# Kernel optimization log

Hardware: AMD Instinct MI355X
Metric: run time of the kernel (lower is better)

## Reference

```python
import jax, jax.numpy as jnp
import numpy as np

N, H, F = 131072, 256, 4096
MIN_FRAG = 3
LN_EPS = 1e-5
NORM_EPS = 1e-12
CONSISTENCY_FACTOR = 0.03
INTERMOLECULAR_WEIGHT = 0.2
SCALING_FACTOR = 0.05  # initial_strength at epoch 0 (progressive schedule, eval mode)


def _normalize(x):
    # torch F.normalize(p=2, dim=1): x / max(||x||, eps)
    n = jnp.linalg.norm(x, axis=-1, keepdims=True)
    return x / jnp.maximum(n, NORM_EPS)


def _frag_consistency(feat, frag_ids, valid):
    # size-weighted sum of per-fragment mean deviations == mean deviation over valid atoms
    m = valid.astype(feat.dtype)[:, None]
    seg_sum = jax.ops.segment_sum(feat * m, frag_ids, num_segments=F)
    seg_cnt = jax.ops.segment_sum(m, frag_ids, num_segments=F)
    means = seg_sum / jnp.maximum(seg_cnt, 1.0)  # scatter-mean over valid atoms
    sim = jnp.sum(_normalize(feat) * _normalize(means)[frag_ids], axis=-1)  # [N]
    dev = (1.0 - sim) * valid.astype(feat.dtype)
    return jnp.sum(dev) / jnp.maximum(jnp.sum(valid.astype(feat.dtype)), 1.0)


def setup_inputs() -> dict:
    key = jax.random.key(0)
    ks = jax.random.split(key, 8)
    return {
        "scalar_short": jax.random.normal(ks[0], (N, H), jnp.float32),
        "scalar_long": jax.random.normal(ks[1], (N, H), jnp.float32),
        "vector_short": jax.random.normal(ks[2], (N, 3, H), jnp.float32),
        "vector_long": jax.random.normal(ks[3], (N, 3, H), jnp.float32),
        "fragment_ids": jax.random.randint(ks[4], (N,), 0, F, dtype=jnp.int32),
        "ln_gamma": jnp.ones((H,), jnp.float32),
        "ln_beta": jnp.zeros((H,), jnp.float32),
        "W1": jax.random.normal(ks[5], (H, H), jnp.float32) / np.sqrt(H),
        "b1": jnp.zeros((H,), jnp.float32),
        "Wv": jax.random.normal(ks[6], (H, H), jnp.float32) / np.sqrt(H),
    }


def reference(scalar_short, scalar_long, vector_short, vector_long, fragment_ids,
              ln_gamma, ln_beta, W1, b1, Wv):
    # valid_mask: atoms belonging to fragments of size >= MIN_FRAG
    sizes = jax.ops.segment_sum(jnp.ones((N,), jnp.float32), fragment_ids, num_segments=F)
    valid = sizes[fragment_ids] >= MIN_FRAG  # [N] bool

    # scalar_projector: LayerNorm -> Linear -> SiLU (dropout identity at eval)
    mu = jnp.mean(scalar_short, axis=-1, keepdims=True)
    var = jnp.var(scalar_short, axis=-1, keepdims=True)
    xh = (scalar_short - mu) / jnp.sqrt(var + LN_EPS) * ln_gamma + ln_beta
    scalar_features = jax.nn.silu(xh @ W1.T + b1)  # [N, H]

    intra = _frag_consistency(scalar_features, fragment_ids, valid)

    # vector branch: per-atom magnitude = mean over 3 spatial comps of ||.||_2 over hidden
    vec_mag = jnp.mean(jnp.linalg.norm(vector_short, axis=2), axis=1, keepdims=True)  # [N,1]
    # Linear(bias=False) on mag.expand(-1,H) then [:, :1] == silu(mag * sum(Wv[0,:]))
    w0 = jnp.sum(Wv[0])
    vector_features = jax.nn.silu(vec_mag * w0)  # [N,1]
    vec_loss = _frag_consistency(vector_features, fragment_ids, valid)

    # interfragment differentiation over ALL atoms (no valid mask)
    cnt = jax.ops.segment_sum(jnp.ones((N, 1), jnp.float32), fragment_ids, num_segments=F)
    sfrag = jax.ops.segment_sum(scalar_features, fragment_ids, num_segments=F) / jnp.maximum(cnt, 1.0)
    vfrag = jax.ops.segment_sum(vec_mag, fragment_ids, num_segments=F) / jnp.maximum(cnt, 1.0)
    combined = _normalize(jnp.concatenate([sfrag, vfrag], axis=1))  # [F, H+1]
    sim = combined @ combined.T  # [F, F]
    off_sum = jnp.sum(sim) - jnp.trace(sim)
    inter = off_sum / (F * F - F + 1e-6)

    total = intra + vec_loss + INTERMOLECULAR_WEIGHT * inter
    return CONSISTENCY_FACTOR * total * SCALING_FACTOR
```

## Files before the change

kernel.cpp:

```cpp
#include <hip/hip_runtime.h>
#include <hip/hip_bf16.h>
#include <stdint.h>

#define NA 131072
#define HD 256
#define NF 4096
#define MINFRAG 3
#define LN_EPS 1e-5f
#define NEPS 1e-12f

#define OFF_CNT    0ull
#define OFF_VSUM   16384ull
#define OFF_VFSUM  32768ull
#define OFF_NVSUM  49152ull
#define OFF_FILL   65536ull
#define OFF_DBL    81920ull
#define OFF_SSUM   86016ull
#define OFF_NSUM   4280320ull
#define ZERO_BYTES 8474624ull
#define OFF_OFFS   8474624ull
#define OFF_SVEC   8491008ull
#define OFF_C0     8492032ull
#define OFF_W0     8493056ull
#define OFF_GBF    8493568ull
#define OFF_ORDER  8624640ull

#define IDX_TRACE 257
#define IDX_DEVS  258
#define IDX_DEVV  259
#define IDX_VCNT  260

typedef __attribute__((ext_vector_type(8))) short short8;
typedef __attribute__((ext_vector_type(4))) float f32x4;
union F4S8 { float4 f; short8 s; };
union BFU { __hip_bfloat16 b; unsigned short u; };

__device__ __forceinline__ unsigned short f2b(float x) {
    BFU t; t.b = __float2bfloat16(x); return t.u;
}
__device__ __forceinline__ float b2f(unsigned short u) {
    return __uint_as_float(((uint32_t)u) << 16);
}
__device__ __forceinline__ float silu_f(float x) { return x / (1.f + expf(-x)); }

__global__ __launch_bounds__(256) void k_prep(
    const float* __restrict__ W1, const float* __restrict__ gamma,
    const float* __restrict__ beta, const float* __restrict__ b1,
    const float* __restrict__ Wv,
    unsigned short* __restrict__ Gbf, float* __restrict__ svec,
    float* __restrict__ c0, float* __restrict__ w0) {
    __shared__ float red[8];
    int o = blockIdx.x;
    int t = threadIdx.x;
    if (o < HD) {
        float w = W1[(size_t)o * HD + t];
        unsigned short gb = f2b(w * gamma[t]);
        Gbf[(size_t)o * HD + t] = gb;
        float sp = b2f(gb);
        float cp = w * beta[t];
#pragma unroll
        for (int m = 32; m; m >>= 1) { sp += __shfl_xor(sp, m, 64); cp += __shfl_xor(cp, m, 64); }
        int wv = t >> 6;
        if ((t & 63) == 0) { red[wv] = sp; red[4 + wv] = cp; }
        __syncthreads();
        if (t == 0) {
            svec[o] = red[0] + red[1] + red[2] + red[3];
            c0[o]   = red[4] + red[5] + red[6] + red[7] + b1[o];
        }
    } else {
        float v = Wv[t];
#pragma unroll
        for (int m = 32; m; m >>= 1) v += __shfl_xor(v, m, 64);
        int wv = t >> 6;
        if ((t & 63) == 0) red[wv] = v;
        __syncthreads();
        if (t == 0) w0[0] = red[0] + red[1] + red[2] + red[3];
    }
}

__global__ __launch_bounds__(256) void k_stats(
    const float* __restrict__ vs, const int* __restrict__ fid,
    const float* __restrict__ w0p,
    int* __restrict__ cnt, float* __restrict__ vsum,
    float* __restrict__ vfsum, float* __restrict__ nvsum) {
    int gwave = (blockIdx.x * blockDim.x + threadIdx.x) >> 6;
    int lane = threadIdx.x & 63;
    int nw = (gridDim.x * blockDim.x) >> 6;
    float w0 = w0p[0];
    for (int i = gwave; i < NA; i += nw) {
        const float* base = vs + (size_t)i * 3 * HD;
        float4 v0 = ((const float4*)(base))[lane];
        float4 v1 = ((const float4*)(base + HD))[lane];
        float4 v2 = ((const float4*)(base + 2 * HD))[lane];
        float q0 = v0.x * v0.x + v0.y * v0.y + v0.z * v0.z + v0.w * v0.w;
        float q1 = v1.x * v1.x + v1.y * v1.y + v1.z * v1.z + v1.w * v1.w;
        float q2 = v2.x * v2.x + v2.y * v2.y + v2.z * v2.z + v2.w * v2.w;
#pragma unroll
        for (int m = 32; m; m >>= 1) {
            q0 += __shfl_xor(q0, m, 64);
            q1 += __shfl_xor(q1, m, 64);
            q2 += __shfl_xor(q2, m, 64);
        }
        if (lane == 0) {
            float vm = (sqrtf(q0) + sqrtf(q1) + sqrtf(q2)) * (1.f / 3.f);
            float vf = silu_f(vm * w0);
            float nv = vf / fmaxf(fabsf(vf), NEPS);
            int f = fid[i];
            atomicAdd(&cnt[f], 1);
            atomicAdd(&vsum[f], vm);
            atomicAdd(&vfsum[f], vf);
            atomicAdd(&nvsum[f], nv);
        }
    }
}

__global__ __launch_bounds__(256) void k_scan(const int* __restrict__ cnt,
                                              int* __restrict__ offs) {
    __shared__ int wsum[4];
    int t = threadIdx.x;
    int base = t * 16;
    int c[16];
    int tot = 0;
#pragma unroll
    for (int j = 0; j < 16; ++j) { c[j] = cnt[base + j]; tot += c[j]; }
    int lane = t & 63, w = t >> 6;
    int v = tot;
#pragma unroll
    for (int d = 1; d < 64; d <<= 1) {
        int o = __shfl_up(v, d, 64);
        if (lane >= d) v += o;
    }
    if (lane == 63) wsum[w] = v;
    __syncthreads();
    int wbase = 0;
    for (int i = 0; i < w; ++i) wbase += wsum[i];
    int run = wbase + v - tot;
#pragma unroll
    for (int j = 0; j < 16; ++j) { offs[base + j] = run; run += c[j]; }
}

__global__ __launch_bounds__(256) void k_scatter(
    const int* __restrict__ fid, const int* __restrict__ offs,
    int* __restrict__ fill, int* __restrict__ order) {
    int i = blockIdx.x * blockDim.x + threadIdx.x;
    if (i < NA) {
        int f = fid[i];
        int p = atomicAdd(&fill[f], 1);
        order[offs[f] + p] = i;
    }
}

__global__ __launch_bounds__(256) void k_gemm(
    const float* __restrict__ A, const unsigned short* __restrict__ Gbf,
    const float* __restrict__ svec, const float* __restrict__ c0,
    const int* __restrict__ order, const int* __restrict__ fid,
    const int* __restrict__ offs, const int* __restrict__ cnt,
    float* __restrict__ ssum, float* __restrict__ nsum) {
    __shared__ float4 As16[64 * 8];
    __shared__ float4 Bs16[256 * 8];
    __shared__ float muS[64], rsS[64], rnS[64];
    __shared__ float sqL[64][4];
    __shared__ int fragS[64];

    int tid = threadIdx.x;
    int lane = tid & 63, wid = tid >> 6;
    int r0 = blockIdx.x * 64;
    int rowT = tid >> 4;
    int c4 = tid & 15;

    if (tid < 64) {
        int gi = order[r0 + tid];
        muS[tid] = __int_as_float(gi);
        fragS[tid] = fid[gi];
    }
    __syncthreads();
    int rid[4];
#pragma unroll
    for (int p = 0; p < 4; ++p) rid[p] = __float_as_int(muS[16 * p + rowT]);
    __syncthreads();

    f32x4 acc[4][4] = {};
    float s1p[4] = {0, 0, 0, 0}, s2p[4] = {0, 0, 0, 0};

    for (int k0 = 0; k0 < HD; k0 += 64) {
#pragma unroll
        for (int p = 0; p < 4; ++p) {
            int row = 16 * p + rowT;
            float4 v = *(const float4*)(A + (size_t)rid[p] * HD + k0 + c4 * 4);
            s1p[p] += v.x + v.y + v.z + v.w;
            s2p[p] += v.x * v.x + v.y * v.y + v.z * v.z + v.w * v.w;
            ushort4 pk;
            pk.x = f2b(v.x); pk.y = f2b(v.y); pk.z = f2b(v.z); pk.w = f2b(v.w);
            int slot = row * 8 + ((c4 >> 1) ^ (row & 7));
            ((ushort4*)&As16[slot])[c4 & 1] = pk;
        }
#pragma unroll
        for (int p = 0; p < 8; ++p) {
            int u = p * 256 + tid;
            int n = u >> 3, cc = u & 7;
            float4 g = *(const float4*)(Gbf + (size_t)n * HD + k0 + cc * 8);
            Bs16[n * 8 + (cc ^ (n & 7))] = g;
        }
        __syncthreads();
#pragma unroll
        for (int kk = 0; kk < 2; ++kk) {
            int uo = kk * 4 + (lane >> 4);
            short8 a[4], b[4];
#pragma unroll
            for (int mi = 0; mi < 4; ++mi) {
                int r = mi * 16 + (lane & 15);
                F4S8 t_; t_.f = As16[r * 8 + (uo ^ (r & 7))];
                a[mi] = t_.s;
            }
#pragma unroll
            for (int ni = 0; ni < 4; ++ni) {
                int n = wid * 64 + ni * 16 + (lane & 15);
                F4S8 t_; t_.f = Bs16[n * 8 + (uo ^ (n & 7))];
                b[ni] = t_.s;
            }
#pragma unroll
            for (int mi = 0; mi < 4; ++mi)
#pragma unroll
                for (int ni = 0; ni < 4; ++ni)
                    acc[mi][ni] = __builtin_amdgcn_mfma_f32_16x16x32_bf16(
                        a[mi], b[ni], acc[mi][ni], 0, 0, 0);
        }
        __syncthreads();
    }
#pragma unroll
    for (int p = 0; p < 4; ++p) {
        float s1 = s1p[p], s2 = s2p[p];
#pragma unroll
        for (int m = 1; m < 16; m <<= 1) {
            s1 += __shfl_xor(s1, m, 64);
            s2 += __shfl_xor(s2, m, 64);
        }
        if (c4 == 0) {
            int row = 16 * p + rowT;
            float mu_ = s1 * (1.f / HD);
            float var = s2 * (1.f / HD) - mu_ * mu_;
            muS[row] = mu_;
            rsS[row] = rsqrtf(var + LN_EPS);
        }
    }
    __syncthreads();
    float sv[4], cv[4];
#pragma unroll
    for (int ni = 0; ni < 4; ++ni) {
        int c = wid * 64 + ni * 16 + (lane & 15);
        sv[ni] = svec[c];
        cv[ni] = c0[c];
    }
    unsigned short* featS = (unsigned short*)Bs16;
    float sq[4][4];
#pragma unroll
    for (int mi = 0; mi < 4; ++mi)
#pragma unroll
        for (int q = 0; q < 4; ++q) {
            int rl = mi * 16 + (lane >> 4) * 4 + q;
            float mu_ = muS[rl], rs_ = rsS[rl];
            float sqa = 0.f;
#pragma unroll
            for (int ni = 0; ni < 4; ++ni) {
                int c = wid * 64 + ni * 16 + (lane & 15);
                float pre = rs_ * (acc[mi][ni][q] - mu_ * sv[ni]) + cv[ni];
                unsigned short us = f2b(silu_f(pre));
                featS[rl * 256 + (c ^ ((rl & 7) << 2))] = us;
                float fr = b2f(us);
                sqa += fr * fr;
            }
            sq[mi][q] = sqa;
        }
#pragma unroll
    for (int mi = 0; mi < 4; ++mi)
#pragma unroll
        for (int q = 0; q < 4; ++q) {
            float s_ = sq[mi][q];
            s_ += __shfl_xor(s_, 1, 64);
            s_ += __shfl_xor(s_, 2, 64);
            s_ += __shfl_xor(s_, 4, 64);
            s_ += __shfl_xor(s_, 8, 64);
            if ((lane & 15) == 0) sqL[mi * 16 + (lane >> 4) * 4 + q][wid] = s_;
        }
    __syncthreads();
    if (tid < 64) {
        float t = sqL[tid][0] + sqL[tid][1] + sqL[tid][2] + sqL[tid][3];
        rnS[tid] = 1.f / fmaxf(sqrtf(t), NEPS);
    }
    __syncthreads();
    int cc = wid * 64 + lane;
    float sAcc = 0.f, nAcc = 0.f;
    int curF = fragS[0];
    for (int row = 0; row < 64; ++row) {
        int f = fragS[row];
        if (f != curF) {
            int gs = offs[curF], n = cnt[curF];
            if (gs >= r0 && gs + n <= r0 + 64) {
                ssum[(size_t)curF * HD + cc] = sAcc;
                nsum[(size_t)curF * HD + cc] = nAcc;
            } else {
                atomicAdd(&ssum[(size_t)curF * HD + cc], sAcc);
                atomicAdd(&nsum[(size_t)curF * HD + cc], nAcc);
            }
            sAcc = 0.f; nAcc = 0.f; curF = f;
        }
        float v = b2f(featS[row * 256 + (cc ^ ((row & 7) << 2))]);
        sAcc += v;
        nAcc = fmaf(v, rnS[row], nAcc);
    }
    {
        int gs = offs[curF], n = cnt[curF];
        if (gs >= r0 && gs + n <= r0 + 64) {
            ssum[(size_t)curF * HD + cc] = sAcc;
            nsum[(size_t)curF * HD + cc] = nAcc;
        } else {
            atomicAdd(&ssum[(size_t)curF * HD + cc], sAcc);
            atomicAdd(&nsum[(size_t)curF * HD + cc], nAcc);
        }
    }
}

__global__ __launch_bounds__(256) void k_frag(
    const float* __restrict__ ssum, const float* __restrict__ nsum,
    const int* __restrict__ cnt, const float* __restrict__ vsum,
    const float* __restrict__ vfsum, const float* __restrict__ nvsum,
    double* __restrict__ dbl) {
    int gwave = (blockIdx.x * blockDim.x + threadIdx.x) >> 6;
    int lane = threadIdx.x & 63;
    int nw = (gridDim.x * blockDim.x) >> 6;

    double la0 = 0, la1 = 0, la2 = 0, la3 = 0;
    double lv = 0, ltr = 0, lvc = 0, ldS = 0, ldV = 0;

    for (int f = gwave; f < NF; f += nw) {
        float4 s = ((const float4*)(ssum + (size_t)f * HD))[lane];
        float4 nn = ((const float4*)(nsum + (size_t)f * HD))[lane];
        int c = cnt[f];
        float ssq = s.x * s.x + s.y * s.y + s.z * s.z + s.w * s.w;
        float dsn = nn.x * s.x + nn.y * s.y + nn.z * s.z + nn.w * s.w;
#pragma unroll
        for (int m = 32; m; m >>= 1) {
            ssq += __shfl_xor(ssq, m, 64);
            dsn += __shfl_xor(dsn, m, 64);
        }
        float inv_all = 1.f / fmaxf((float)c, 1.f);
        float m0 = s.x * inv_all, m1 = s.y * inv_all, m2 = s.z * inv_all, m3 = s.w * inv_all;
        float ssq_mean = ssq * inv_all * inv_all;
        float vfr = vsum[f] * inv_all;
        float nrm2 = ssq_mean + vfr * vfr;
        float inv = 1.f / fmaxf(sqrtf(nrm2), NEPS);
        la0 += (double)(m0 * inv);
        la1 += (double)(m1 * inv);
        la2 += (double)(m2 * inv);
        la3 += (double)(m3 * inv);
        if (lane == 0) {
            lv += (double)(vfr * inv);
            ltr += (double)(nrm2 * inv * inv);
            if (c >= MINFRAG) {
                lvc += (double)c;
                float denom = fmaxf(sqrtf(ssq), NEPS);
                ldS += (double)c - (double)(dsn / denom);
                float vfm = vfsum[f] * inv_all;
                float vsgn = vfm / fmaxf(fabsf(vfm), NEPS);
                ldV += (double)c - (double)(vsgn * nvsum[f]);
            }
        }
    }
    atomicAdd(&dbl[4 * lane + 0], la0);
    atomicAdd(&dbl[4 * lane + 1], la1);
    atomicAdd(&dbl[4 * lane + 2], la2);
    atomicAdd(&dbl[4 * lane + 3], la3);
    if (lane == 0) {
        atomicAdd(&dbl[256], lv);
        atomicAdd(&dbl[IDX_TRACE], ltr);
        atomicAdd(&dbl[IDX_VCNT], lvc);
        atomicAdd(&dbl[IDX_DEVS], ldS);
        atomicAdd(&dbl[IDX_DEVV], ldV);
    }
}

__global__ __launch_bounds__(64) void k_final(const double* __restrict__ dbl,
                                              float* __restrict__ out) {
    if (threadIdx.x == 0 && blockIdx.x == 0) {
        double s2 = 0;
        for (int d = 0; d < 257; ++d) s2 += dbl[d] * dbl[d];
        double off = s2 - dbl[IDX_TRACE];
        double inter = off / ((double)NF * NF - NF + 1e-6);
        double vc = fmax(dbl[IDX_VCNT], 1.0);
        double total = dbl[IDX_DEVS] / vc + dbl[IDX_DEVV] / vc + 0.2 * inter;
        out[0] = (float)(0.03 * 0.05 * total);
    }
}

extern "C" void kernel_launch(void* const* d_in, const int* in_sizes, int n_in,
                              void* d_out, int out_size, void* d_ws, size_t ws_size,
                              hipStream_t stream) {
    const float* scalar_short = (const float*)d_in[0];
    const float* vector_short = (const float*)d_in[2];
    const int* fragment_ids = (const int*)d_in[4];
    const float* ln_gamma = (const float*)d_in[5];
    const float* ln_beta = (const float*)d_in[6];
    const float* W1 = (const float*)d_in[7];
    const float* b1 = (const float*)d_in[8];
    const float* Wv = (const float*)d_in[9];
    float* out = (float*)d_out;

    char* ws = (char*)d_ws;
    int* cnt = (int*)(ws + OFF_CNT);
    float* vsum = (float*)(ws + OFF_VSUM);
    float* vfsum = (float*)(ws + OFF_VFSUM);
    float* nvsum = (float*)(ws + OFF_NVSUM);
    int* fill = (int*)(ws + OFF_FILL);
    double* dbl = (double*)(ws + OFF_DBL);
    float* ssum = (float*)(ws + OFF_SSUM);
    float* nsum = (float*)(ws + OFF_NSUM);
    int* offs = (int*)(ws + OFF_OFFS);
    float* svec = (float*)(ws + OFF_SVEC);
    float* c0 = (float*)(ws + OFF_C0);
    float* w0 = (float*)(ws + OFF_W0);
    unsigned short* Gbf = (unsigned short*)(ws + OFF_GBF);
    int* order = (int*)(ws + OFF_ORDER);

    hipMemsetAsync(ws, 0, ZERO_BYTES, stream);
    k_prep<<<HD + 1, 256, 0, stream>>>(W1, ln_gamma, ln_beta, b1, Wv, Gbf, svec, c0, w0);
    k_stats<<<2048, 256, 0, stream>>>(vector_short, fragment_ids, w0, cnt, vsum, vfsum, nvsum);
    k_scan<<<1, 256, 0, stream>>>(cnt, offs);
    k_scatter<<<NA / 256, 256, 0, stream>>>(fragment_ids, offs, fill, order);
    k_gemm<<<NA / 64, 256, 0, stream>>>(scalar_short, Gbf, svec, c0, order,
                                        fragment_ids, offs, cnt, ssum, nsum);
    k_frag<<<64, 256, 0, stream>>>(ssum, nsum, cnt, vsum, vfsum, nvsum, dbl);
    k_final<<<1, 64, 0, stream>>>(dbl, out);
}
```

Measured before the change: 252.7 us.

## Fuse vector-magnitude stats into sorted GEMM and drop large memset

The separate pass over vector_short that computed per-atom magnitudes and per-fragment sums is folded into the GEMM kernel. Each block now reads its fragment-sorted atoms' vector rows alongside the scalar tile, so that streaming overlaps with MFMA work and one launch goes away. The GEMM tile grows to 128 rows with 512 threads. W1·gamma is pre-swizzled into the shared-memory layout so the B tile loads become straight vector copies. Zeroing of the large ssum/nsum buffers moves from a memset into a new histogram kernel, which now also builds the fragment counts. In exchange the fused kernel has higher register and shared-memory pressure, and the vector rows are gathered in sorted order instead of read sequentially.

Result: slower. 292.6 us (+15.8%).

```diff
diff --git a/kernel.cpp b/kernel.cpp
--- a/kernel.cpp
+++ b/kernel.cpp
@@ -15,15 +15,15 @@
 #define OFF_NVSUM  49152ull
 #define OFF_FILL   65536ull
 #define OFF_DBL    81920ull
-#define OFF_SSUM   86016ull
-#define OFF_NSUM   4280320ull
-#define ZERO_BYTES 8474624ull
-#define OFF_OFFS   8474624ull
-#define OFF_SVEC   8491008ull
-#define OFF_C0     8492032ull
-#define OFF_W0     8493056ull
-#define OFF_GBF    8493568ull
-#define OFF_ORDER  8624640ull
+#define ZERO_HEAD  84224ull
+#define OFF_OFFS   86016ull
+#define OFF_SVEC   102400ull
+#define OFF_C0     103424ull
+#define OFF_W0     104448ull
+#define OFF_GBF    106496ull
+#define OFF_ORDER  237568ull
+#define OFF_SSUM   761856ull
+#define OFF_NSUM   4956160ull
 
 #define IDX_TRACE 257
 #define IDX_DEVS  258
@@ -47,7 +47,7 @@
     const float* __restrict__ W1, const float* __restrict__ gamma,
     const float* __restrict__ beta, const float* __restrict__ b1,
     const float* __restrict__ Wv,
-    unsigned short* __restrict__ Gbf, float* __restrict__ svec,
+    unsigned short* __restrict__ GbfArr, float* __restrict__ svec,
     float* __restrict__ c0, float* __restrict__ w0) {
     __shared__ float red[8];
     int o = blockIdx.x;
@@ -55,7 +55,8 @@
     if (o < HD) {
         float w = W1[(size_t)o * HD + t];
         unsigned short gb = f2b(w * gamma[t]);
-        Gbf[(size_t)o * HD + t] = gb;
+        int kc = t >> 6, cc = (t >> 3) & 7, klo = t & 7;
+        GbfArr[(size_t)kc * 16384 + (o * 8 + (cc ^ (o & 7))) * 8 + klo] = gb;
         float sp = b2f(gb);
         float cp = w * beta[t];
 #pragma unroll
@@ -78,40 +79,12 @@
     }
 }
 
-__global__ __launch_bounds__(256) void k_stats(
-    const float* __restrict__ vs, const int* __restrict__ fid,
-    const float* __restrict__ w0p,
-    int* __restrict__ cnt, float* __restrict__ vsum,
-    float* __restrict__ vfsum, float* __restrict__ nvsum) {
-    int gwave = (blockIdx.x * blockDim.x + threadIdx.x) >> 6;
-    int lane = threadIdx.x & 63;
-    int nw = (gridDim.x * blockDim.x) >> 6;
-    float w0 = w0p[0];
-    for (int i = gwave; i < NA; i += nw) {
-        const float* base = vs + (size_t)i * 3 * HD;
-        float4 v0 = ((const float4*)(base))[lane];
-        float4 v1 = ((const float4*)(base + HD))[lane];
-        float4 v2 = ((const float4*)(base + 2 * HD))[lane];
-        float q0 = v0.x * v0.x + v0.y * v0.y + v0.z * v0.z + v0.w * v0.w;
-        float q1 = v1.x * v1.x + v1.y * v1.y + v1.z * v1.z + v1.w * v1.w;
-        float q2 = v2.x * v2.x + v2.y * v2.y + v2.z * v2.z + v2.w * v2.w;
-#pragma unroll
-        for (int m = 32; m; m >>= 1) {
-            q0 += __shfl_xor(q0, m, 64);
-            q1 += __shfl_xor(q1, m, 64);
-            q2 += __shfl_xor(q2, m, 64);
-        }
-        if (lane == 0) {
-            float vm = (sqrtf(q0) + sqrtf(q1) + sqrtf(q2)) * (1.f / 3.f);
-            float vf = silu_f(vm * w0);
-            float nv = vf / fmaxf(fabsf(vf), NEPS);
-            int f = fid[i];
-            atomicAdd(&cnt[f], 1);
-            atomicAdd(&vsum[f], vm);
-            atomicAdd(&vfsum[f], vf);
-            atomicAdd(&nvsum[f], nv);
-        }
-    }
+__global__ __launch_bounds__(256) void k_hist(
+    const int* __restrict__ fid, int* __restrict__ cnt, float4* __restrict__ zbuf) {
+    int i = blockIdx.x * 256 + threadIdx.x;
+    float4 z = {0.f, 0.f, 0.f, 0.f};
+    zbuf[i] = z;
+    if (i < NA) atomicAdd(&cnt[fid[i]], 1);
 }
 
 __global__ __launch_bounds__(256) void k_scan(const int* __restrict__ cnt,
@@ -150,56 +123,84 @@
     }
 }
 
-__global__ __launch_bounds__(256) void k_gemm(
-    const float* __restrict__ A, const unsigned short* __restrict__ Gbf,
+#define BM 128
+__global__ __launch_bounds__(512, 2) void k_gemm(
+    const float* __restrict__ A, const unsigned short* __restrict__ GbfArr,
     const float* __restrict__ svec, const float* __restrict__ c0,
+    const float* __restrict__ vs, const float* __restrict__ w0p,
     const int* __restrict__ order, const int* __restrict__ fid,
     const int* __restrict__ offs, const int* __restrict__ cnt,
+    float* __restrict__ vsum, float* __restrict__ vfsum, float* __restrict__ nvsum,
     float* __restrict__ ssum, float* __restrict__ nsum) {
-    __shared__ float4 As16[64 * 8];
-    __shared__ float4 Bs16[256 * 8];
-    __shared__ float muS[64], rsS[64], rnS[64];
-    __shared__ float sqL[64][4];
-    __shared__ int fragS[64];
+    __shared__ char U[65536];
+    __shared__ float muS[BM], rsS[BM], rnS[BM];
+    __shared__ float sqL[BM][4];
+    __shared__ int ridS[BM], fragS[BM];
+
+    float4* As = (float4*)U;
+    float4* Bs = (float4*)(U + 16384);
+    unsigned short* featS = (unsigned short*)U;
 
     int tid = threadIdx.x;
     int lane = tid & 63, wid = tid >> 6;
-    int r0 = blockIdx.x * 64;
-    int rowT = tid >> 4;
-    int c4 = tid & 15;
-
-    if (tid < 64) {
+    int wr = wid >> 2, wc = wid & 3;
+    int r0 = blockIdx.x * BM;
+    int rowA = tid >> 2, sub = tid & 3;
+    float w0 = w0p[0];
+
+    if (tid < BM) {
         int gi = order[r0 + tid];
-        muS[tid] = __int_as_float(gi);
+        ridS[tid] = gi;
         fragS[tid] = fid[gi];
     }
     __syncthreads();
-    int rid[4];
-#pragma unroll
-    for (int p = 0; p < 4; ++p) rid[p] = __float_as_int(muS[16 * p + rowT]);
-    __syncthreads();
 
     f32x4 acc[4][4] = {};
-    float s1p[4] = {0, 0, 0, 0}, s2p[4] = {0, 0, 0, 0};
-
-    for (int k0 = 0; k0 < HD; k0 += 64) {
+    float s1 = 0.f, s2 = 0.f;
+    const float* Ap = A + (size_t)ridS[rowA] * HD + sub * 16;
+
+    for (int kc = 0; kc < 4; ++kc) {
 #pragma unroll
         for (int p = 0; p < 4; ++p) {
-            int row = 16 * p + rowT;
-            float4 v = *(const float4*)(A + (size_t)rid[p] * HD + k0 + c4 * 4);
-            s1p[p] += v.x + v.y + v.z + v.w;
-            s2p[p] += v.x * v.x + v.y * v.y + v.z * v.z + v.w * v.w;
+            int idx = p * 512 + tid;
+            Bs[idx] = *(const float4*)(GbfArr + (size_t)kc * 16384 + (size_t)idx * 8);
+        }
+#pragma unroll
+        for (int q = 0; q < 4; ++q) {
+            int f4 = sub * 4 + q;
+            float4 v = *(const float4*)(Ap + kc * 64 + q * 4);
+            s1 += v.x + v.y + v.z + v.w;
+            s2 += v.x * v.x + v.y * v.y + v.z * v.z + v.w * v.w;
             ushort4 pk;
             pk.x = f2b(v.x); pk.y = f2b(v.y); pk.z = f2b(v.z); pk.w = f2b(v.w);
-            int slot = row * 8 + ((c4 >> 1) ^ (row & 7));
-            ((ushort4*)&As16[slot])[c4 & 1] = pk;
-        }
-#pragma unroll
-        for (int p = 0; p < 8; ++p) {
-            int u = p * 256 + tid;
-            int n = u >> 3, cc = u & 7;
-            float4 g = *(const float4*)(Gbf + (size_t)n * HD + k0 + cc * 8);
-            Bs16[n * 8 + (cc ^ (n & 7))] = g;
+            ((ushort4*)&As[rowA * 8 + ((f4 >> 1) ^ (rowA & 7))])[f4 & 1] = pk;
+        }
+#pragma unroll
+        for (int j = 0; j < 4; ++j) {
+            int lr = kc * 32 + wid * 4 + j;
+            int gi = ridS[lr];
+            const float* vb = vs + (size_t)gi * 3 * HD;
+            float4 v0 = ((const float4*)vb)[lane];
+            float4 v1 = ((const float4*)(vb + HD))[lane];
+            float4 v2 = ((const float4*)(vb + 2 * HD))[lane];
+            float q0 = v0.x * v0.x + v0.y * v0.y + v0.z * v0.z + v0.w * v0.w;
+            float q1 = v1.x * v1.x + v1.y * v1.y + v1.z * v1.z + v1.w * v1.w;
+            float q2 = v2.x * v2.x + v2.y * v2.y + v2.z * v2.z + v2.w * v2.w;
+#pragma unroll
+            for (int m = 32; m; m >>= 1) {
+                q0 += __shfl_xor(q0, m, 64);
+                q1 += __shfl_xor(q1, m, 64);
+                q2 += __shfl_xor(q2, m, 64);
+            }
+            if (lane == 0) {
+                float vm = (sqrtf(q0) + sqrtf(q1) + sqrtf(q2)) * (1.f / 3.f);
+                float vf = silu_f(vm * w0);
+                float nv = vf / fmaxf(fabsf(vf), NEPS);
+                int f = fragS[lr];
+                atomicAdd(&vsum[f], vm);
+                atomicAdd(&vfsum[f], vf);
+                atomicAdd(&nvsum[f], nv);
+            }
         }
         __syncthreads();
 #pragma unroll
@@ -208,14 +209,14 @@
             short8 a[4], b[4];
 #pragma unroll
             for (int mi = 0; mi < 4; ++mi) {
-                int r = mi * 16 + (lane & 15);
-                F4S8 t_; t_.f = As16[r * 8 + (uo ^ (r & 7))];
+                int r = wr * 64 + mi * 16 + (lane & 15);
+                F4S8 t_; t_.f = As[r * 8 + (uo ^ (r & 7))];
                 a[mi] = t_.s;
             }
 #pragma unroll
             for (int ni = 0; ni < 4; ++ni) {
-                int n = wid * 64 + ni * 16 + (lane & 15);
-                F4S8 t_; t_.f = Bs16[n * 8 + (uo ^ (n & 7))];
+                int n = wc * 64 + ni * 16 + (lane & 15);
+                F4S8 t_; t_.f = Bs[n * 8 + (uo ^ (n & 7))];
                 b[ni] = t_.s;
             }
 #pragma unroll
@@ -227,42 +228,33 @@
         }
         __syncthreads();
     }
-#pragma unroll
-    for (int p = 0; p < 4; ++p) {
-        float s1 = s1p[p], s2 = s2p[p];
-#pragma unroll
-        for (int m = 1; m < 16; m <<= 1) {
-            s1 += __shfl_xor(s1, m, 64);
-            s2 += __shfl_xor(s2, m, 64);
-        }
-        if (c4 == 0) {
-            int row = 16 * p + rowT;
-            float mu_ = s1 * (1.f / HD);
-            float var = s2 * (1.f / HD) - mu_ * mu_;
-            muS[row] = mu_;
-            rsS[row] = rsqrtf(var + LN_EPS);
-        }
+    s1 += __shfl_xor(s1, 1, 64); s1 += __shfl_xor(s1, 2, 64);
+    s2 += __shfl_xor(s2, 1, 64); s2 += __shfl_xor(s2, 2, 64);
+    if (sub == 0) {
+        float mu_ = s1 * (1.f / HD);
+        float var = s2 * (1.f / HD) - mu_ * mu_;
+        muS[rowA] = mu_;
+        rsS[rowA] = rsqrtf(var + LN_EPS);
     }
     __syncthreads();
     float sv[4], cv[4];
 #pragma unroll
     for (int ni = 0; ni < 4; ++ni) {
-        int c = wid * 64 + ni * 16 + (lane & 15);
+        int c = wc * 64 + ni * 16 + (lane & 15);
         sv[ni] = svec[c];
         cv[ni] = c0[c];
     }
-    unsigned short* featS = (unsigned short*)Bs16;
     float sq[4][4];
 #pragma unroll
     for (int mi = 0; mi < 4; ++mi)
 #pragma unroll
         for (int q = 0; q < 4; ++q) {
-            int rl = mi * 16 + (lane >> 4) * 4 + q;
+            int rl = wr * 64 + mi * 16 + (lane >> 4) * 4 + q;
             float mu_ = muS[rl], rs_ = rsS[rl];
             float sqa = 0.f;
 #pragma unroll
             for (int ni = 0; ni < 4; ++ni) {
-                int c = wid * 64 + ni * 16 + (lane & 15);
+                int c = wc * 64 + ni * 16 + (lane & 15);
                 float pre = rs_ * (acc[mi][ni][q] - mu_ * sv[ni]) + cv[ni];
                 unsigned short us = f2b(silu_f(pre));
                 featS[rl * 256 + (c ^ ((rl & 7) << 2))] = us;
@@ -280,42 +272,44 @@
             s_ += __shfl_xor(s_, 2, 64);
             s_ += __shfl_xor(s_, 4, 64);
             s_ += __shfl_xor(s_, 8, 64);
-            if ((lane & 15) == 0) sqL[mi * 16 + (lane >> 4) * 4 + q][wid] = s_;
+            if ((lane & 15) == 0) sqL[wr * 64 + mi * 16 + (lane >> 4) * 4 + q][wc] = s_;
         }
     __syncthreads();
-    if (tid < 64) {
+    if (tid < BM) {
         float t = sqL[tid][0] + sqL[tid][1] + sqL[tid][2] + sqL[tid][3];
         rnS[tid] = 1.f / fmaxf(sqrtf(t), NEPS);
     }
     __syncthreads();
-    int cc = wid * 64 + lane;
+    int half = tid >> 8, c = tid & 255;
+    int rbase = r0 + half * 64;
     float sAcc = 0.f, nAcc = 0.f;
-    int curF = fragS[0];
-    for (int row = 0; row < 64; ++row) {
+    int curF = fragS[half * 64];
+    for (int j = 0; j < 64; ++j) {
+        int row = half * 64 + j;
         int f = fragS[row];
         if (f != curF) {
             int gs = offs[curF], n = cnt[curF];
-            if (gs >= r0 && gs + n <= r0 + 64) {
-                ssum[(size_t)curF * HD + cc] = sAcc;
-                nsum[(size_t)curF * HD + cc] = nAcc;
+            if (gs >= rbase && gs + n <= rbase + 64) {
+                ssum[(size_t)curF * HD + c] = sAcc;
+                nsum[(size_t)curF * HD + c] = nAcc;
             } else {
-                atomicAdd(&ssum[(size_t)curF * HD + cc], sAcc);
-                atomicAdd(&nsum[(size_t)curF * HD + cc], nAcc);
+                atomicAdd(&ssum[(size_t)curF * HD + c], sAcc);
+                atomicAdd(&nsum[(size_t)curF * HD + c], nAcc);
             }
             sAcc = 0.f; nAcc = 0.f; curF = f;
         }
-        float v = b2f(featS[row * 256 + (cc ^ ((row & 7) << 2))]);
+        float v = b2f(featS[row * 256 + (c ^ ((row & 7) << 2))]);
         sAcc += v;
         nAcc = fmaf(v, rnS[row], nAcc);
     }
     {
         int gs = offs[curF], n = cnt[curF];
-        if (gs >= r0 && gs + n <= r0 + 64) {
-            ssum[(size_t)curF * HD + cc] = sAcc;
-            nsum[(size_t)curF * HD + cc] = nAcc;
+        if (gs >= rbase && gs + n <= rbase + 64) {
+            ssum[(size_t)curF * HD + c] = sAcc;
+            nsum[(size_t)curF * HD + c] = nAcc;
         } else {
-            atomicAdd(&ssum[(size_t)curF * HD + cc], sAcc);
-            atomicAdd(&nsum[(size_t)curF * HD + cc], nAcc);
+            atomicAdd(&ssum[(size_t)curF * HD + c], sAcc);
+            atomicAdd(&nsum[(size_t)curF * HD + c], nAcc);
         }
     }
 }
@@ -412,22 +406,23 @@
     float* nvsum = (float*)(ws + OFF_NVSUM);
     int* fill = (int*)(ws + OFF_FILL);
     double* dbl = (double*)(ws + OFF_DBL);
-    float* ssum = (float*)(ws + OFF_SSUM);
-    float* nsum = (float*)(ws + OFF_NSUM);
     int* offs = (int*)(ws + OFF_OFFS);
     float* svec = (float*)(ws + OFF_SVEC);
     float* c0 = (float*)(ws + OFF_C0);
     float* w0 = (float*)(ws + OFF_W0);
-    unsigned short* Gbf = (unsigned short*)(ws + OFF_GBF);
+    unsigned short* GbfArr = (unsigned short*)(ws + OFF_GBF);
     int* order = (int*)(ws + OFF_ORDER);
-
-    hipMemsetAsync(ws, 0, ZERO_BYTES, stream);
-    k_prep<<<HD + 1, 256, 0, stream>>>(W1, ln_gamma, ln_beta, b1, Wv, Gbf, svec, c0, w0);
-    k_stats<<<2048, 256, 0, stream>>>(vector_short, fragment_ids, w0, cnt, vsum, vfsum, nvsum);
+    float* ssum = (float*)(ws + OFF_SSUM);
+    float* nsum = (float*)(ws + OFF_NSUM);
+
+    hipMemsetAsync(ws, 0, ZERO_HEAD, stream);
+    k_prep<<<HD + 1, 256, 0, stream>>>(W1, ln_gamma, ln_beta, b1, Wv, GbfArr, svec, c0, w0);
+    k_hist<<<2048, 256, 0, stream>>>(fragment_ids, cnt, (float4*)(ws + OFF_SSUM));
     k_scan<<<1, 256, 0, stream>>>(cnt, offs);
     k_scatter<<<NA / 256, 256, 0, stream>>>(fragment_ids, offs, fill, order);
-    k_gemm<<<NA / 64, 256, 0, stream>>>(scalar_short, Gbf, svec, c0, order,
-                                        fragment_ids, offs, cnt, ssum, nsum);
+    k_gemm<<<NA / BM, 512, 0, stream>>>(scalar_short, GbfArr, svec, c0,
+                                        vector_short, w0, order, fragment_ids,
+                                        offs, cnt, vsum, vfsum, nvsum, ssum, nsum);
     k_frag<<<64, 256, 0, stream>>>(ssum, nsum, cnt, vsum, vfsum, nvsum, dbl);
     k_final<<<1, 64, 0, stream>>>(dbl, out);
 }
```

## Fuse vector stats into GEMM kernel as side role; split histogram; pre-swizzle weights

Applied to the files above, without the earlier changes.

The vector-magnitude statistics pass (reads 1.5 GB-scale vector_short) moves out of its own kernel and runs as a third block role interleaved inside the GEMM launch, so its memory streaming overlaps the MFMA work. A small histogram kernel now computes fragment counts and also zeroes the ssum/nsum buffers, which shrinks the memset to the header. The bf16 weight matrix is stored pre-swizzled per k-chunk, so the GEMM's B-tile load becomes a straight contiguous copy. The risk is that role blocks compete for bandwidth and CUs, with possible imbalance between roles.

Result: slower. 296.6 us (+17.4%).

```diff
diff --git a/kernel.cpp b/kernel.cpp
--- a/kernel.cpp
+++ b/kernel.cpp
@@ -15,15 +15,15 @@
 #define OFF_NVSUM  49152ull
 #define OFF_FILL   65536ull
 #define OFF_DBL    81920ull
-#define OFF_SSUM   86016ull
-#define OFF_NSUM   4280320ull
-#define ZERO_BYTES 8474624ull
-#define OFF_OFFS   8474624ull
-#define OFF_SVEC   8491008ull
-#define OFF_C0     8492032ull
-#define OFF_W0     8493056ull
-#define OFF_GBF    8493568ull
-#define OFF_ORDER  8624640ull
+#define ZERO_HEAD  84224ull
+#define OFF_OFFS   86016ull
+#define OFF_SVEC   102400ull
+#define OFF_C0     103424ull
+#define OFF_W0     104448ull
+#define OFF_GBF    106496ull
+#define OFF_ORDER  237568ull
+#define OFF_SSUM   761856ull
+#define OFF_NSUM   4956160ull
 
 #define IDX_TRACE 257
 #define IDX_DEVS  258
@@ -47,7 +47,7 @@
     const float* __restrict__ W1, const float* __restrict__ gamma,
     const float* __restrict__ beta, const float* __restrict__ b1,
     const float* __restrict__ Wv,
-    unsigned short* __restrict__ Gbf, float* __restrict__ svec,
+    unsigned short* __restrict__ GbfArr, float* __restrict__ svec,
     float* __restrict__ c0, float* __restrict__ w0) {
     __shared__ float red[8];
     int o = blockIdx.x;
@@ -55,7 +55,8 @@
     if (o < HD) {
         float w = W1[(size_t)o * HD + t];
         unsigned short gb = f2b(w * gamma[t]);
-        Gbf[(size_t)o * HD + t] = gb;
+        int kc = t >> 6, cc = (t >> 3) & 7, klo = t & 7;
+        GbfArr[(size_t)kc * 16384 + (size_t)(o * 8 + (cc ^ (o & 7))) * 8 + klo] = gb;
         float sp = b2f(gb);
         float cp = w * beta[t];
 #pragma unroll
@@ -78,40 +79,12 @@
     }
 }
 
-__global__ __launch_bounds__(256) void k_stats(
-    const float* __restrict__ vs, const int* __restrict__ fid,
-    const float* __restrict__ w0p,
-    int* __restrict__ cnt, float* __restrict__ vsum,
-    float* __restrict__ vfsum, float* __restrict__ nvsum) {
-    int gwave = (blockIdx.x * blockDim.x + threadIdx.x) >> 6;
-    int lane = threadIdx.x & 63;
-    int nw = (gridDim.x * blockDim.x) >> 6;
-    float w0 = w0p[0];
-    for (int i = gwave; i < NA; i += nw) {
-        const float* base = vs + (size_t)i * 3 * HD;
-        float4 v0 = ((const float4*)(base))[lane];
-        float4 v1 = ((const float4*)(base + HD))[lane];
-        float4 v2 = ((const float4*)(base + 2 * HD))[lane];
-        float q0 = v0.x * v0.x + v0.y * v0.y + v0.z * v0.z + v0.w * v0.w;
-        float q1 = v1.x * v1.x + v1.y * v1.y + v1.z * v1.z + v1.w * v1.w;
-        float q2 = v2.x * v2.x + v2.y * v2.y + v2.z * v2.z + v2.w * v2.w;
-#pragma unroll
-        for (int m = 32; m; m >>= 1) {
-            q0 += __shfl_xor(q0, m, 64);
-            q1 += __shfl_xor(q1, m, 64);
-            q2 += __shfl_xor(q2, m, 64);
-        }
-        if (lane == 0) {
-            float vm = (sqrtf(q0) + sqrtf(q1) + sqrtf(q2)) * (1.f / 3.f);
-            float vf = silu_f(vm * w0);
-            float nv = vf / fmaxf(fabsf(vf), NEPS);
-            int f = fid[i];
-            atomicAdd(&cnt[f], 1);
-            atomicAdd(&vsum[f], vm);
-            atomicAdd(&vfsum[f], vf);
-            atomicAdd(&nvsum[f], nv);
-        }
-    }
+__global__ __launch_bounds__(256) void k_hist(
+    const int* __restrict__ fid, int* __restrict__ cnt, float4* __restrict__ zbuf) {
+    int i = blockIdx.x * 256 + threadIdx.x;
+    float4 z = {0.f, 0.f, 0.f, 0.f};
+    zbuf[i] = z;
+    if (i < NA) atomicAdd(&cnt[fid[i]], 1);
 }
 
 __global__ __launch_bounds__(256) void k_scan(const int* __restrict__ cnt,
@@ -150,11 +123,13 @@
     }
 }
 
-__global__ __launch_bounds__(256) void k_gemm(
-    const float* __restrict__ A, const unsigned short* __restrict__ Gbf,
+__global__ __launch_bounds__(256) void k_main(
+    const float* __restrict__ A, const unsigned short* __restrict__ GbfArr,
     const float* __restrict__ svec, const float* __restrict__ c0,
+    const float* __restrict__ vs, const float* __restrict__ w0p,
     const int* __restrict__ order, const int* __restrict__ fid,
     const int* __restrict__ offs, const int* __restrict__ cnt,
+    float* __restrict__ vsum, float* __restrict__ vfsum, float* __restrict__ nvsum,
     float* __restrict__ ssum, float* __restrict__ nsum) {
     __shared__ float4 As16[64 * 8];
     __shared__ float4 Bs16[256 * 8];
@@ -164,7 +139,44 @@
 
     int tid = threadIdx.x;
     int lane = tid & 63, wid = tid >> 6;
-    int r0 = blockIdx.x * 64;
+    int b = blockIdx.x;
+    int role = b % 3;
+
+    if (role == 2) {
+        int sid = b / 3;
+        int g4 = sid * 4 + wid;
+        int i0 = g4 * 32;
+        float w0 = w0p[0];
+        for (int j = 0; j < 32; ++j) {
+            int i = i0 + j;
+            const float* vb = vs + (size_t)i * 3 * HD;
+            float4 v0 = ((const float4*)vb)[lane];
+            float4 v1 = ((const float4*)(vb + HD))[lane];
+            float4 v2 = ((const float4*)(vb + 2 * HD))[lane];
+            float q0 = v0.x * v0.x + v0.y * v0.y + v0.z * v0.z + v0.w * v0.w;
+            float q1 = v1.x * v1.x + v1.y * v1.y + v1.z * v1.z + v1.w * v1.w;
+            float q2 = v2.x * v2.x + v2.y * v2.y + v2.z * v2.z + v2.w * v2.w;
+#pragma unroll
+            for (int m = 32; m; m >>= 1) {
+                q0 += __shfl_xor(q0, m, 64);
+                q1 += __shfl_xor(q1, m, 64);
+                q2 += __shfl_xor(q2, m, 64);
+            }
+            if (lane == 0) {
+                float vm = (sqrtf(q0) + sqrtf(q1) + sqrtf(q2)) * (1.f / 3.f);
+                float vf = silu_f(vm * w0);
+                float nv = vf / fmaxf(fabsf(vf), NEPS);
+                int f = fid[i];
+                atomicAdd(&vsum[f], vm);
+                atomicAdd(&vfsum[f], vf);
+                atomicAdd(&nvsum[f], nv);
+            }
+        }
+        return;
+    }
+
+    int gb = (b / 3) * 2 + role;
+    int r0 = gb * 64;
     int rowT = tid >> 4;
     int c4 = tid & 15;
 
@@ -182,7 +194,8 @@
     f32x4 acc[4][4] = {};
     float s1p[4] = {0, 0, 0, 0}, s2p[4] = {0, 0, 0, 0};
 
-    for (int k0 = 0; k0 < HD; k0 += 64) {
+    for (int kc = 0; kc < 4; ++kc) {
+        int k0 = kc * 64;
 #pragma unroll
         for (int p = 0; p < 4; ++p) {
             int row = 16 * p + rowT;
@@ -196,16 +209,14 @@
         }
 #pragma unroll
         for (int p = 0; p < 8; ++p) {
-            int u = p * 256 + tid;
-            int n = u >> 3, cc = u & 7;
-            float4 g = *(const float4*)(Gbf + (size_t)n * HD + k0 + cc * 8);
-            Bs16[n * 8 + (cc ^ (n & 7))] = g;
+            int idx = p * 256 + tid;
+            Bs16[idx] = ((const float4*)(GbfArr + (size_t)kc * 16384))[idx];
         }
         __syncthreads();
 #pragma unroll
         for (int kk = 0; kk < 2; ++kk) {
             int uo = kk * 4 + (lane >> 4);
-            short8 a[4], b[4];
+            short8 a[4], bfr[4];
 #pragma unroll
             for (int mi = 0; mi < 4; ++mi) {
                 int r = mi * 16 + (lane & 15);
@@ -216,14 +227,14 @@
             for (int ni = 0; ni < 4; ++ni) {
                 int n = wid * 64 + ni * 16 + (lane & 15);
                 F4S8 t_; t_.f = Bs16[n * 8 + (uo ^ (n & 7))];
-                b[ni] = t_.s;
+                bfr[ni] = t_.s;
             }
 #pragma unroll
             for (int mi = 0; mi < 4; ++mi)
 #pragma unroll
                 for (int ni = 0; ni < 4; ++ni)
                     acc[mi][ni] = __builtin_amdgcn_mfma_f32_16x16x32_bf16(
-                        a[mi], b[ni], acc[mi][ni], 0, 0, 0);
+                        a[mi], bfr[ni], acc[mi][ni], 0, 0, 0);
         }
         __syncthreads();
     }
@@ -412,22 +423,23 @@
     float* nvsum = (float*)(ws + OFF_NVSUM);
     int* fill = (int*)(ws + OFF_FILL);
     double* dbl = (double*)(ws + OFF_DBL);
-    float* ssum = (float*)(ws + OFF_SSUM);
-    float* nsum = (float*)(ws + OFF_NSUM);
     int* offs = (int*)(ws + OFF_OFFS);
     float* svec = (float*)(ws + OFF_SVEC);
     float* c0 = (float*)(ws + OFF_C0);
     float* w0 = (float*)(ws + OFF_W0);
-    unsigned short* Gbf = (unsigned short*)(ws + OFF_GBF);
+    unsigned short* GbfArr = (unsigned short*)(ws + OFF_GBF);
     int* order = (int*)(ws + OFF_ORDER);
-
-    hipMemsetAsync(ws, 0, ZERO_BYTES, stream);
-    k_prep<<<HD + 1, 256, 0, stream>>>(W1, ln_gamma, ln_beta, b1, Wv, Gbf, svec, c0, w0);
-    k_stats<<<2048, 256, 0, stream>>>(vector_short, fragment_ids, w0, cnt, vsum, vfsum, nvsum);
+    float* ssum = (float*)(ws + OFF_SSUM);
+    float* nsum = (float*)(ws + OFF_NSUM);
+
+    hipMemsetAsync(ws, 0, ZERO_HEAD, stream);
+    k_prep<<<HD + 1, 256, 0, stream>>>(W1, ln_gamma, ln_beta, b1, Wv, GbfArr, svec, c0, w0);
+    k_hist<<<2048, 256, 0, stream>>>(fragment_ids, cnt, (float4*)(ws + OFF_SSUM));
     k_scan<<<1, 256, 0, stream>>>(cnt, offs);
     k_scatter<<<NA / 256, 256, 0, stream>>>(fragment_ids, offs, fill, order);
-    k_gemm<<<NA / 64, 256, 0, stream>>>(scalar_short, Gbf, svec, c0, order,
-                                        fragment_ids, offs, cnt, ssum, nsum);
+    k_main<<<3072, 256, 0, stream>>>(scalar_short, GbfArr, svec, c0,
+                                     vector_short, w0, order, fragment_ids,
+                                     offs, cnt, vsum, vfsum, nvsum, ssum, nsum);
     k_frag<<<64, 256, 0, stream>>>(ssum, nsum, cnt, vsum, vfsum, nvsum, dbl);
     k_final<<<1, 64, 0, stream>>>(dbl, out);
 }
```

## Preload full A tile once per block, split histogram from vector stats, custom zero kernel

Applied to the files above, without the earlier changes.

The GEMM kernel now loads each block's 64 gathered rows in full (all 256 columns) into a larger shared buffer up front and computes the LayerNorm statistics there. This replaces the per-k-chunk A loads interleaved with B loads and the separate reduction pass, giving more independent loads in flight and fewer syncs, at the cost of 32KB of shared memory for A. The fragment count histogram moves out of k_stats into a lightweight k_hist kernel so the scan and scatter no longer wait behind the large vector_short pass. hipMemsetAsync is replaced by a custom zeroing kernel.

New measurement: 268.7 us. 6.4% more time.

```diff
diff --git a/kernel.cpp b/kernel.cpp
--- a/kernel.cpp
+++ b/kernel.cpp
@@ -43,6 +43,12 @@
 }
 __device__ __forceinline__ float silu_f(float x) { return x / (1.f + expf(-x)); }
 
+__global__ __launch_bounds__(256) void k_zero(float4* __restrict__ z) {
+    int i = blockIdx.x * 256 + threadIdx.x;
+    float4 v = {0.f, 0.f, 0.f, 0.f};
+    z[i] = v;
+}
+
 __global__ __launch_bounds__(256) void k_prep(
     const float* __restrict__ W1, const float* __restrict__ gamma,
     const float* __restrict__ beta, const float* __restrict__ b1,
@@ -78,11 +84,53 @@
     }
 }
 
+__global__ __launch_bounds__(256) void k_hist(
+    const int* __restrict__ fid, int* __restrict__ cnt) {
+    int i = blockIdx.x * 256 + threadIdx.x;
+    if (i < NA) atomicAdd(&cnt[fid[i]], 1);
+}
+
+__global__ __launch_bounds__(256) void k_scan(const int* __restrict__ cnt,
+                                              int* __restrict__ offs) {
+    __shared__ int wsum[4];
+    int t = threadIdx.x;
+    int base = t * 16;
+    int c[16];
+    int tot = 0;
+#pragma unroll
+    for (int j = 0; j < 16; ++j) { c[j] = cnt[base + j]; tot += c[j]; }
+    int lane = t & 63, w = t >> 6;
+    int v = tot;
+#pragma unroll
+    for (int d = 1; d < 64; d <<= 1) {
+        int o = __shfl_up(v, d, 64);
+        if (lane >= d) v += o;
+    }
+    if (lane == 63) wsum[w] = v;
+    __syncthreads();
+    int wbase = 0;
+    for (int i = 0; i < w; ++i) wbase += wsum[i];
+    int run = wbase + v - tot;
+#pragma unroll
+    for (int j = 0; j < 16; ++j) { offs[base + j] = run; run += c[j]; }
+}
+
+__global__ __launch_bounds__(256) void k_scatter(
+    const int* __restrict__ fid, const int* __restrict__ offs,
+    int* __restrict__ fill, int* __restrict__ order) {
+    int i = blockIdx.x * blockDim.x + threadIdx.x;
+    if (i < NA) {
+        int f = fid[i];
+        int p = atomicAdd(&fill[f], 1);
+        order[offs[f] + p] = i;
+    }
+}
+
 __global__ __launch_bounds__(256) void k_stats(
     const float* __restrict__ vs, const int* __restrict__ fid,
     const float* __restrict__ w0p,
-    int* __restrict__ cnt, float* __restrict__ vsum,
-    float* __restrict__ vfsum, float* __restrict__ nvsum) {
+    float* __restrict__ vsum, float* __restrict__ vfsum,
+    float* __restrict__ nvsum) {
     int gwave = (blockIdx.x * blockDim.x + threadIdx.x) >> 6;
     int lane = threadIdx.x & 63;
     int nw = (gridDim.x * blockDim.x) >> 6;
@@ -106,47 +154,10 @@
             float vf = silu_f(vm * w0);
             float nv = vf / fmaxf(fabsf(vf), NEPS);
             int f = fid[i];
-            atomicAdd(&cnt[f], 1);
             atomicAdd(&vsum[f], vm);
             atomicAdd(&vfsum[f], vf);
             atomicAdd(&nvsum[f], nv);
         }
-    }
-}
-
-__global__ __launch_bounds__(256) void k_scan(const int* __restrict__ cnt,
-                                              int* __restrict__ offs) {
-    __shared__ int wsum[4];
-    int t = threadIdx.x;
-    int base = t * 16;
-    int c[16];
-    int tot = 0;
-#pragma unroll
-    for (int j = 0; j < 16; ++j) { c[j] = cnt[base + j]; tot += c[j]; }
-    int lane = t & 63, w = t >> 6;
-    int v = tot;
-#pragma unroll
-    for (int d = 1; d < 64; d <<= 1) {
-        int o = __shfl_up(v, d, 64);
-        if (lane >= d) v += o;
-    }
-    if (lane == 63) wsum[w] = v;
-    __syncthreads();
-    int wbase = 0;
-    for (int i = 0; i < w; ++i) wbase += wsum[i];
-    int run = wbase + v - tot;
-#pragma unroll
-    for (int j = 0; j < 16; ++j) { offs[base + j] = run; run += c[j]; }
-}
-
-__global__ __launch_bounds__(256) void k_scatter(
-    const int* __restrict__ fid, const int* __restrict__ offs,
-    int* __restrict__ fill, int* __restrict__ order) {
-    int i = blockIdx.x * blockDim.x + threadIdx.x;
-    if (i < NA) {
-        int f = fid[i];
-        int p = atomicAdd(&fill[f], 1);
-        order[offs[f] + p] = i;
     }
 }
 
@@ -156,94 +167,81 @@
     const int* __restrict__ order, const int* __restrict__ fid,
     const int* __restrict__ offs, const int* __restrict__ cnt,
     float* __restrict__ ssum, float* __restrict__ nsum) {
-    __shared__ float4 As16[64 * 8];
+    __shared__ float4 As16[64 * 32];
     __shared__ float4 Bs16[256 * 8];
     __shared__ float muS[64], rsS[64], rnS[64];
     __shared__ float sqL[64][4];
-    __shared__ int fragS[64];
+    __shared__ int ridS[64], fragS[64];
 
     int tid = threadIdx.x;
     int lane = tid & 63, wid = tid >> 6;
     int r0 = blockIdx.x * 64;
-    int rowT = tid >> 4;
-    int c4 = tid & 15;
 
     if (tid < 64) {
         int gi = order[r0 + tid];
-        muS[tid] = __int_as_float(gi);
+        ridS[tid] = gi;
         fragS[tid] = fid[gi];
     }
     __syncthreads();
-    int rid[4];
-#pragma unroll
-    for (int p = 0; p < 4; ++p) rid[p] = __float_as_int(muS[16 * p + rowT]);
-    __syncthreads();
+
+    int rowA = tid >> 2, qa = tid & 3;
+    const float4* Ap = (const float4*)(A + (size_t)ridS[rowA] * HD + qa * 64);
+    float s1 = 0.f, s2 = 0.f;
+#pragma unroll
+    for (int j = 0; j < 16; ++j) {
+        float4 v = Ap[j];
+        s1 += v.x + v.y + v.z + v.w;
+        s2 += v.x * v.x + v.y * v.y + v.z * v.z + v.w * v.w;
+        ushort4 pk;
+        pk.x = f2b(v.x); pk.y = f2b(v.y); pk.z = f2b(v.z); pk.w = f2b(v.w);
+        ((ushort4*)&As16[qa * 512 + rowA * 8 + ((j >> 1) ^ (rowA & 7))])[j & 1] = pk;
+    }
+    s1 += __shfl_xor(s1, 1, 64); s1 += __shfl_xor(s1, 2, 64);
+    s2 += __shfl_xor(s2, 1, 64); s2 += __shfl_xor(s2, 2, 64);
+    if (qa == 0) {
+        float mu_ = s1 * (1.f / HD);
+        float var = s2 * (1.f / HD) - mu_ * mu_;
+        muS[rowA] = mu_;
+        rsS[rowA] = rsqrtf(var + LN_EPS);
+    }
 
     f32x4 acc[4][4] = {};
-    float s1p[4] = {0, 0, 0, 0}, s2p[4] = {0, 0, 0, 0};
-
-    for (int k0 = 0; k0 < HD; k0 += 64) {
-#pragma unroll
-        for (int p = 0; p < 4; ++p) {
-            int row = 16 * p + rowT;
-            float4 v = *(const float4*)(A + (size_t)rid[p] * HD + k0 + c4 * 4);
-            s1p[p] += v.x + v.y + v.z + v.w;
-            s2p[p] += v.x * v.x + v.y * v.y + v.z * v.z + v.w * v.w;
-            ushort4 pk;
-            pk.x = f2b(v.x); pk.y = f2b(v.y); pk.z = f2b(v.z); pk.w = f2b(v.w);
-            int slot = row * 8 + ((c4 >> 1) ^ (row & 7));
-            ((ushort4*)&As16[slot])[c4 & 1] = pk;
-        }
+
+    for (int kc = 0; kc < 4; ++kc) {
 #pragma unroll
         for (int p = 0; p < 8; ++p) {
             int u = p * 256 + tid;
             int n = u >> 3, cc = u & 7;
-            float4 g = *(const float4*)(Gbf + (size_t)n * HD + k0 + cc * 8);
+            float4 g = *(const float4*)(Gbf + (size_t)n * HD + kc * 64 + cc * 8);
             Bs16[n * 8 + (cc ^ (n & 7))] = g;
         }
         __syncthreads();
 #pragma unroll
         for (int kk = 0; kk < 2; ++kk) {
             int uo = kk * 4 + (lane >> 4);
-            short8 a[4], b[4];
+            short8 a[4], bfr[4];
 #pragma unroll
             for (int mi = 0; mi < 4; ++mi) {
                 int r = mi * 16 + (lane & 15);
-                F4S8 t_; t_.f = As16[r * 8 + (uo ^ (r & 7))];
+                F4S8 t_; t_.f = As16[kc * 512 + r * 8 + (uo ^ (r & 7))];
                 a[mi] = t_.s;
             }
 #pragma unroll
             for (int ni = 0; ni < 4; ++ni) {
                 int n = wid * 64 + ni * 16 + (lane & 15);
                 F4S8 t_; t_.f = Bs16[n * 8 + (uo ^ (n & 7))];
-                b[ni] = t_.s;
+                bfr[ni] = t_.s;
             }
 #pragma unroll
             for (int mi = 0; mi < 4; ++mi)
 #pragma unroll
                 for (int ni = 0; ni < 4; ++ni)
                     acc[mi][ni] = __builtin_amdgcn_mfma_f32_16x16x32_bf16(
-                        a[mi], b[ni], acc[mi][ni], 0, 0, 0);
+                        a[mi], bfr[ni], acc[mi][ni], 0, 0, 0);
         }
         __syncthreads();
     }
-#pragma unroll
-    for (int p = 0; p < 4; ++p) {
-        float s1 = s1p[p], s2 = s2p[p];
-#pragma unroll
-        for (int m = 1; m < 16; m <<= 1) {
-            s1 += __shfl_xor(s1, m, 64);
-            s2 += __shfl_xor(s2, m, 64);
-        }
-        if (c4 == 0) {
-            int row = 16 * p + rowT;
-            float mu_ = s1 * (1.f / HD);
-            float var = s2 * (1.f / HD) - mu_ * mu_;
-            muS[row] = mu_;
-            rsS[row] = rsqrtf(var + LN_EPS);
-        }
-    }
-    __syncthreads();
+
     float sv[4], cv[4];
 #pragma unroll
     for (int ni = 0; ni < 4; ++ni) {
@@ -421,11 +419,12 @@
     unsigned short* Gbf = (unsigned short*)(ws + OFF_GBF);
     int* order = (int*)(ws + OFF_ORDER);
 
-    hipMemsetAsync(ws, 0, ZERO_BYTES, stream);
+    k_zero<<<2069, 256, 0, stream>>>((float4*)ws);
     k_prep<<<HD + 1, 256, 0, stream>>>(W1, ln_gamma, ln_beta, b1, Wv, Gbf, svec, c0, w0);
-    k_stats<<<2048, 256, 0, stream>>>(vector_short, fragment_ids, w0, cnt, vsum, vfsum, nvsum);
+    k_hist<<<NA / 256, 256, 0, stream>>>(fragment_ids, cnt);
     k_scan<<<1, 256, 0, stream>>>(cnt, offs);
     k_scatter<<<NA / 256, 256, 0, stream>>>(fragment_ids, offs, fill, order);
+    k_stats<<<2048, 256, 0, stream>>>(vector_short, fragment_ids, w0, vsum, vfsum, nvsum);
     k_gemm<<<NA / 64, 256, 0, stream>>>(scalar_short, Gbf, svec, c0, order,
                                         fragment_ids, offs, cnt, ssum, nsum);
     k_frag<<<64, 256, 0, stream>>>(ssum, nsum, cnt, vsum, vfsum, nvsum, dbl);
```
